# Optimization experiments

Measured on AMD Instinct MI355X. Metric: run time of the kernel, lower is better.

The kernel has to match this reference:

```python
import jax, jax.numpy as jnp
import numpy as np

N = 50000
E = 800000
F_IN = 512
H = 128
K = 10
ALPHA = 0.1
EPS = 1e-5  # BatchNorm eps


def setup_inputs() -> dict:
    key = jax.random.key(0)
    ks = jax.random.split(key, 16)
    x = jax.random.normal(ks[0], (N, F_IN), dtype=jnp.float32)
    edge_index = jax.random.randint(ks[1], (2, E), 0, N, dtype=jnp.int64)
    # Linear weights (xavier-ish scale)
    W1 = jax.random.normal(ks[2], (F_IN, H), dtype=jnp.float32) * (1.0 / np.sqrt(F_IN))
    b1 = jnp.zeros((H,), dtype=jnp.float32)
    W2 = jax.random.normal(ks[3], (H, H), dtype=jnp.float32) * (1.0 / np.sqrt(H))
    b2 = jnp.zeros((H,), dtype=jnp.float32)
    # BatchNorm (eval mode: running stats)
    gamma1 = jnp.ones((H,), dtype=jnp.float32)
    beta1 = jnp.zeros((H,), dtype=jnp.float32)
    mean1 = jax.random.normal(ks[4], (H,), dtype=jnp.float32) * 0.1
    var1 = jax.random.uniform(ks[5], (H,), dtype=jnp.float32) + 0.5
    gamma2 = jnp.ones((H,), dtype=jnp.float32)
    beta2 = jnp.zeros((H,), dtype=jnp.float32)
    mean2 = jax.random.normal(ks[6], (H,), dtype=jnp.float32) * 0.1
    var2 = jax.random.uniform(ks[7], (H,), dtype=jnp.float32) + 0.5
    return {
        "x": x, "edge_index": edge_index,
        "W1": W1, "b1": b1, "gamma1": gamma1, "beta1": beta1, "mean1": mean1, "var1": var1,
        "W2": W2, "b2": b2, "gamma2": gamma2, "beta2": beta2, "mean2": mean2, "var2": var2,
    }


def _bn_eval(h, gamma, beta, mean, var):
    return (h - mean) * jax.lax.rsqrt(var + EPS) * gamma + beta


def _appnp_prop(h, edge_index):
    # add self loops
    loop = jnp.arange(N, dtype=edge_index.dtype)
    src = jnp.concatenate([edge_index[0], loop])
    dst = jnp.concatenate([edge_index[1], loop])
    # symmetric GCN normalization: deg^{-1/2}[src] * deg^{-1/2}[dst]
    deg = jax.ops.segment_sum(jnp.ones_like(src, dtype=h.dtype), dst, num_segments=N)
    dinv = jax.lax.rsqrt(jnp.maximum(deg, 1.0))
    norm = dinv[src] * dinv[dst]  # [E+N]
    h0 = h

    def step(carry, _):
        msg = carry[src] * norm[:, None]                    # [E+N, H]
        agg = jax.ops.segment_sum(msg, dst, num_segments=N)  # [N, H]
        return (1.0 - ALPHA) * agg + ALPHA * h0, None

    out, _ = jax.lax.scan(step, h, None, length=K)
    return out


def reference(x, edge_index, W1, b1, gamma1, beta1, mean1, var1,
              W2, b2, gamma2, beta2, mean2, var2):
    h = jax.nn.relu(x @ W1 + b1)
    h = _bn_eval(h, gamma1, beta1, mean1, var1)
    # dropout inactive (eval mode)
    h = h @ W2 + b2
    h = _bn_eval(h, gamma2, beta2, mean2, var2)
    return _appnp_prop(h, edge_index)
```

## Files before the change

kernel.cpp:

```cpp
#include <hip/hip_runtime.h>

#define ALPHA_F 0.1f
#define EPS_F   1e-5f

typedef float    f32x4 __attribute__((ext_vector_type(4)));
typedef _Float16 h16x8 __attribute__((ext_vector_type(8)));
typedef _Float16 h16x2 __attribute__((ext_vector_type(2)));

__device__ __forceinline__ void gll16(const void* g, void* l)
{
    __builtin_amdgcn_global_load_lds(
        (const __attribute__((address_space(1))) void*)g,
        (__attribute__((address_space(3))) void*)l, 16, 0, 0);
}

__device__ __forceinline__ int pad_cnt(int d) { return (d + 8) & ~7; }

__global__ void convert_wstg(const float* __restrict__ W,
                             _Float16* __restrict__ Wstg, int K)
{
    int idx = blockIdx.x * 256 + threadIdx.x;
    if (idx < K * 128) {
        int k = idx >> 7, n = idx & 127;
        int i = k >> 5, kg = (k >> 3) & 3, j = k & 7;
        Wstg[(size_t)i * 4096 + (kg * 128 + n) * 8 + j] = (_Float16)W[idx];
    }
}

template<bool A_HALF, bool OUT_HALF>
__global__ __launch_bounds__(256) void gemm_stage_bn(
    const void* __restrict__ Av,
    const _Float16* __restrict__ Wstg,
    const float* __restrict__ bias,
    const float* __restrict__ gamma, const float* __restrict__ beta,
    const float* __restrict__ mean,  const float* __restrict__ var,
    void* __restrict__ outv, int M, int K, int do_relu)
{
    __shared__ __align__(16) char Abuf[2][8192];
    __shared__ __align__(16) char Wbuf[2][8192];

    const int t   = threadIdx.x;
    const int w   = t >> 6;
    const int l   = t & 63;
    const int l15 = l & 15;
    const int lk  = l >> 4;
    const int bm  = blockIdx.x * 64;
    const int nk  = K >> 5;
    const int row = w * 16 + l15;

    f32x4 acc[8];
#pragma unroll
    for (int f = 0; f < 8; ++f) acc[f] = (f32x4){0.f, 0.f, 0.f, 0.f};

    auto stage = [&](int buf, int i) {
        const char* wsrc = (const char*)Wstg + (size_t)i * 8192;
#pragma unroll
        for (int c = 0; c < 2; ++c) {
            const int base = w * 128 + c * 64;
            gll16(wsrc + (size_t)(base + l) * 16, &Wbuf[buf][base * 16]);
        }
        if (A_HALF) {
            const int base = w * 64;
            const int sl   = base + l;
            const int r    = sl >> 2;
            const int ch   = (sl & 3) ^ (r & 3);
            int gr = bm + r; gr = (gr < M) ? gr : (M - 1);
            const char* src = (const char*)Av + ((size_t)gr * K + i * 32) * 2
                              + (size_t)ch * 16;
            gll16(src, &Abuf[buf][base * 16]);
        } else {
#pragma unroll
            for (int c = 0; c < 2; ++c) {
                const int base = w * 128 + c * 64;
                const int sl   = base + l;
                const int r    = sl >> 3;
                const int ch   = (sl & 7) ^ (r & 7);
                int gr = bm + r; gr = (gr < M) ? gr : (M - 1);
                const char* src = (const char*)Av + ((size_t)gr * K + i * 32) * 4
                                  + (size_t)ch * 16;
                gll16(src, &Abuf[buf][base * 16]);
            }
        }
    };

    auto compute = [&](int buf) {
        h16x8 a;
        if (A_HALF) {
            a = *(const h16x8*)&Abuf[buf][(row * 4 + (lk ^ (row & 3))) * 16];
        } else {
            f32x4 a0 = *(const f32x4*)&Abuf[buf][(row * 8 + ((2 * lk)     ^ (row & 7))) * 16];
            f32x4 a1 = *(const f32x4*)&Abuf[buf][(row * 8 + ((2 * lk + 1) ^ (row & 7))) * 16];
#pragma unroll
            for (int j = 0; j < 4; ++j) {
                a[j]     = (_Float16)a0[j];
                a[4 + j] = (_Float16)a1[j];
            }
        }
#pragma unroll
        for (int f = 0; f < 8; ++f) {
            h16x8 b = *(const h16x8*)&Wbuf[buf][(lk * 128 + f * 16 + l15) * 16];
            acc[f] = __builtin_amdgcn_mfma_f32_16x16x32_f16(a, b, acc[f], 0, 0, 0);
        }
    };

    stage(0, 0);
    for (int i = 0; i < nk; ++i) {
        __syncthreads();
        if (i + 1 < nk) stage((i + 1) & 1, i + 1);
        compute(i & 1);
    }

#pragma unroll
    for (int f = 0; f < 8; ++f) {
        const int col = f * 16 + l15;
        float s  = gamma[col] * rsqrtf(var[col] + EPS_F);
        float sh = beta[col] - mean[col] * s;
        float bb = bias[col];
#pragma unroll
        for (int rr = 0; rr < 4; ++rr) {
            int rg = bm + w * 16 + lk * 4 + rr;
            if (rg < M) {
                float v = acc[f][rr] + bb;
                if (do_relu) v = fmaxf(v, 0.f);
                v = v * s + sh;
                if (OUT_HALF) ((_Float16*)outv)[(size_t)rg * 128 + col] = (_Float16)v;
                else          ((float*)outv)[(size_t)rg * 128 + col]    = v;
            }
        }
    }
}

__global__ void count_deg(const int* __restrict__ dst, int E, int* __restrict__ deg)
{
    int e = blockIdx.x * 256 + threadIdx.x;
    if (e < E) atomicAdd(&deg[dst[e]], 1);
}

__global__ __launch_bounds__(256) void scan_block_sums(
    const int* __restrict__ deg, int* __restrict__ bsum, int N)
{
    __shared__ int sh[256];
    const int t  = threadIdx.x;
    const int i0 = blockIdx.x * 1024 + t * 4;
    int s = 0;
    if (i0 + 3 < N) {
        int4 d4 = *(const int4*)(deg + i0);
        s = pad_cnt(d4.x) + pad_cnt(d4.y) + pad_cnt(d4.z) + pad_cnt(d4.w);
    } else {
#pragma unroll
        for (int j = 0; j < 4; ++j)
            if (i0 + j < N) s += pad_cnt(deg[i0 + j]);
    }
    sh[t] = s;
    __syncthreads();
#pragma unroll
    for (int d = 128; d > 0; d >>= 1) {
        if (t < d) sh[t] += sh[t + d];
        __syncthreads();
    }
    if (t == 0) bsum[blockIdx.x] = sh[0];
}

__global__ __launch_bounds__(256) void scan_offsets(
    const int* __restrict__ deg, const int* __restrict__ bsum,
    int* __restrict__ offs, int* __restrict__ cursor,
    float* __restrict__ dinv, int N, int B)
{
    __shared__ int sh[256];
    __shared__ int sbase;
    const int b = blockIdx.x, t = threadIdx.x;

    int v = (t < b && t < B) ? bsum[t] : 0;
    sh[t] = v;
    __syncthreads();
#pragma unroll
    for (int d = 128; d > 0; d >>= 1) {
        if (t < d) sh[t] += sh[t + d];
        __syncthreads();
    }
    if (t == 0) sbase = sh[0];
    __syncthreads();

    const int i0 = b * 1024 + t * 4;
    int c[4], s = 0;
#pragma unroll
    for (int j = 0; j < 4; ++j) {
        int i = i0 + j;
        c[j] = (i < N) ? pad_cnt(deg[i]) : 0;
        s += c[j];
    }
    sh[t] = s;
    __syncthreads();
    for (int d = 1; d < 256; d <<= 1) {
        int o = (t >= d) ? sh[t - d] : 0;
        __syncthreads();
        sh[t] += o;
        __syncthreads();
    }
    int run = sbase + sh[t] - s;
#pragma unroll
    for (int j = 0; j < 4; ++j) {
        int i = i0 + j;
        if (i < N) {
            offs[i]   = run;
            cursor[i] = run;
            dinv[i]   = rsqrtf((float)(deg[i] + 1));
            run += c[j];
        }
    }
    if (b == B - 1 && t == 255) offs[N] = run;
}

__global__ void scatter_csr(const int* __restrict__ src, const int* __restrict__ dst,
                            int E, const float* __restrict__ dinv,
                            int* __restrict__ cursor, int2* __restrict__ csr)
{
    int e = blockIdx.x * 256 + threadIdx.x;
    if (e < E) {
        int s = src[e], d = dst[e];
        int pos = atomicAdd(&cursor[d], 1);
        csr[pos] = make_int2(s, __float_as_int(dinv[s] * dinv[d]));
    }
}

__global__ void fill_self_pad(const int* __restrict__ offs, const int* __restrict__ deg,
                              const float* __restrict__ dinv,
                              int2* __restrict__ csr, int N)
{
    int i = blockIdx.x * 256 + threadIdx.x;
    if (i < N) {
        int base = offs[i], d = deg[i], end = offs[i + 1];
        float di = dinv[i];
        csr[base + d] = make_int2(i, __float_as_int(di * di));
        for (int p = base + d + 1; p < end; ++p)
            csr[p] = make_int2(i, 0);
    }
}

#define NWAVES 8192

__global__ __launch_bounds__(256) void appnp_step(
    const _Float16* __restrict__ cur, const _Float16* __restrict__ h0,
    const int* __restrict__ offs, const int2* __restrict__ csr,
    _Float16* __restrict__ nxt, float* __restrict__ fout, int N)
{
    const int wv0  = __builtin_amdgcn_readfirstlane(
                        (int)((blockIdx.x * 256u + threadIdx.x) >> 6));
    const int lane = (int)(threadIdx.x & 63u);
    const int g    = lane >> 4;
    const int fl   = (lane & 15) * 8;

    for (int i = wv0; i < N; i += NWAVES) {
        int e   = offs[i];
        int end = offs[i + 1];

        h16x2 acc[4];
#pragma unroll
        for (int j = 0; j < 4; ++j) acc[j] = (h16x2){(_Float16)0, (_Float16)0};

        int4 m = *(const int4*)(csr + e + 2 * g);
        h16x8 vA = *(const h16x8*)(cur + (size_t)m.x * 128 + fl);
        h16x8 vB = *(const h16x8*)(cur + (size_t)m.z * 128 + fl);

        for (e += 8; e < end; e += 8) {
            int4 m2 = *(const int4*)(csr + e + 2 * g);
            h16x8 vA2 = *(const h16x8*)(cur + (size_t)m2.x * 128 + fl);
            h16x8 vB2 = *(const h16x8*)(cur + (size_t)m2.z * 128 + fl);
            _Float16 ha = (_Float16)__int_as_float(m.y);
            _Float16 hb = (_Float16)__int_as_float(m.w);
            h16x2 wa = (h16x2){ha, ha}, wb = (h16x2){hb, hb};
#pragma unroll
            for (int j = 0; j < 4; ++j) {
                h16x2 va = (h16x2){vA[2 * j], vA[2 * j + 1]};
                h16x2 vb = (h16x2){vB[2 * j], vB[2 * j + 1]};
                acc[j] = __builtin_elementwise_fma(wa, va, acc[j]);
                acc[j] = __builtin_elementwise_fma(wb, vb, acc[j]);
            }
            m = m2; vA = vA2; vB = vB2;
        }
        {
            _Float16 ha = (_Float16)__int_as_float(m.y);
            _Float16 hb = (_Float16)__int_as_float(m.w);
            h16x2 wa = (h16x2){ha, ha}, wb = (h16x2){hb, hb};
#pragma unroll
            for (int j = 0; j < 4; ++j) {
                h16x2 va = (h16x2){vA[2 * j], vA[2 * j + 1]};
                h16x2 vb = (h16x2){vB[2 * j], vB[2 * j + 1]};
                acc[j] = __builtin_elementwise_fma(wa, va, acc[j]);
                acc[j] = __builtin_elementwise_fma(wb, vb, acc[j]);
            }
        }

        float o[8];
#pragma unroll
        for (int j = 0; j < 4; ++j) {
            o[2 * j]     = (float)acc[j][0];
            o[2 * j + 1] = (float)acc[j][1];
        }
#pragma unroll
        for (int j = 0; j < 8; ++j) {
            o[j] += __shfl_xor(o[j], 16);
            o[j] += __shfl_xor(o[j], 32);
        }

        if (lane < 16) {
            h16x8 hv = *(const h16x8*)(h0 + (size_t)i * 128 + fl);
#pragma unroll
            for (int j = 0; j < 8; ++j)
                o[j] = ALPHA_F * (float)hv[j] + (1.f - ALPHA_F) * o[j];
            if (fout) {
                f32x4 o0, o1;
#pragma unroll
                for (int j = 0; j < 4; ++j) { o0[j] = o[j]; o1[j] = o[4 + j]; }
                *(f32x4*)(fout + (size_t)i * 128 + fl)     = o0;
                *(f32x4*)(fout + (size_t)i * 128 + fl + 4) = o1;
            } else {
                h16x8 o16;
#pragma unroll
                for (int j = 0; j < 8; ++j) o16[j] = (_Float16)o[j];
                *(h16x8*)(nxt + (size_t)i * 128 + fl) = o16;
            }
        }
    }
}

static inline size_t align_up(size_t x) { return (x + 255) & ~(size_t)255; }

extern "C" void kernel_launch(void* const* d_in, const int* in_sizes, int n_in,
                              void* d_out, int out_size, void* d_ws, size_t ws_size,
                              hipStream_t stream)
{
    const float* x   = (const float*)d_in[0];
    const int*   ei  = (const int*)d_in[1];
    const float* W1  = (const float*)d_in[2];
    const float* b1  = (const float*)d_in[3];
    const float* g1  = (const float*)d_in[4];
    const float* be1 = (const float*)d_in[5];
    const float* m1  = (const float*)d_in[6];
    const float* v1  = (const float*)d_in[7];
    const float* W2  = (const float*)d_in[8];
    const float* b2  = (const float*)d_in[9];
    const float* g2  = (const float*)d_in[10];
    const float* be2 = (const float*)d_in[11];
    const float* m2  = (const float*)d_in[12];
    const float* v2  = (const float*)d_in[13];

    const int N = in_sizes[0] / 512;
    const int E = in_sizes[1] / 2;
    const int* src = ei;
    const int* dst = ei + E;
    const int CSR_CAP = E + 8 * N;
    const int NB = (N + 1023) / 1024;

    char* ws = (char*)d_ws;
    size_t off = 0;
    _Float16* hAh = (_Float16*)(ws + off); off += align_up((size_t)N * 128 * 2);
    _Float16* h0h = (_Float16*)(ws + off); off += align_up((size_t)N * 128 * 2);
    _Float16* p0  = (_Float16*)(ws + off); off += align_up((size_t)N * 128 * 2);
    _Float16* p1  = (_Float16*)(ws + off); off += align_up((size_t)N * 128 * 2);
    int*    deg  = (int*)(ws + off);    off += align_up((size_t)N * 4);
    float*  dinv = (float*)(ws + off);  off += align_up((size_t)N * 4);
    int*    offs = (int*)(ws + off);    off += align_up((size_t)(N + 1) * 4);
    int*    curs = (int*)(ws + off);    off += align_up((size_t)N * 4);
    int*    bsum = (int*)(ws + off);    off += align_up((size_t)256 * 4);
    int2*   csr  = (int2*)(ws + off);   off += align_up((size_t)CSR_CAP * 8);
    _Float16* w1s = (_Float16*)(ws + off); off += align_up((size_t)512 * 128 * 2);
    _Float16* w2s = (_Float16*)(ws + off); off += align_up((size_t)128 * 128 * 2);

    hipMemsetAsync(deg, 0, (size_t)N * 4, stream);
    count_deg<<<(E + 255) / 256, 256, 0, stream>>>(dst, E, deg);
    scan_block_sums<<<NB, 256, 0, stream>>>(deg, bsum, N);
    scan_offsets<<<NB, 256, 0, stream>>>(deg, bsum, offs, curs, dinv, N, NB);
    scatter_csr<<<(E + 255) / 256, 256, 0, stream>>>(src, dst, E, dinv, curs, csr);
    fill_self_pad<<<(N + 255) / 256, 256, 0, stream>>>(offs, deg, dinv, csr, N);

    convert_wstg<<<(512 * 128 + 255) / 256, 256, 0, stream>>>(W1, w1s, 512);
    convert_wstg<<<(128 * 128 + 255) / 256, 256, 0, stream>>>(W2, w2s, 128);

    gemm_stage_bn<false, true><<<(N + 63) / 64, 256, 0, stream>>>(
        x, w1s, b1, g1, be1, m1, v1, hAh, N, 512, 1);
    gemm_stage_bn<true, true><<<(N + 63) / 64, 256, 0, stream>>>(
        hAh, w2s, b2, g2, be2, m2, v2, h0h, N, 128, 0);

    const _Float16* cur = h0h;
    for (int k = 0; k < 10; ++k) {
        _Float16* nxt = (k & 1) ? p1 : p0;
        float* fo = (k == 9) ? (float*)d_out : nullptr;
        appnp_step<<<NWAVES / 4, 256, 0, stream>>>(
            cur, h0h, offs, csr, nxt, fo, N);
        cur = nxt;
    }

    (void)n_in; (void)out_size; (void)ws_size;
}
```

Before: 430.0 us.

## Store propagation features as packed 12-bit fixed-point to cut gather bandwidth

```diff
diff --git a/kernel.cpp b/kernel.cpp
--- a/kernel.cpp
+++ b/kernel.cpp
@@ -2,10 +2,11 @@
 
 #define ALPHA_F 0.1f
 #define EPS_F   1e-5f
+#define INV256  0.00390625f
 
 typedef float    f32x4 __attribute__((ext_vector_type(4)));
 typedef _Float16 h16x8 __attribute__((ext_vector_type(8)));
-typedef _Float16 h16x2 __attribute__((ext_vector_type(2)));
+typedef int      i32x3 __attribute__((ext_vector_type(3)));
 
 __device__ __forceinline__ void gll16(const void* g, void* l)
 {
@@ -15,6 +16,51 @@
 }
 
 __device__ __forceinline__ int pad_cnt(int d) { return (d + 8) & ~7; }
+
+__device__ __forceinline__ void pack12(const float* o, unsigned* d)
+{
+    int q[8];
+#pragma unroll
+    for (int j = 0; j < 8; ++j) {
+        float x = fminf(fmaxf(o[j] * 256.f, -2047.f), 2047.f);
+        q[j] = (int)lrintf(x) & 0xFFF;
+    }
+    d[0] = (unsigned)q[0] | ((unsigned)q[1] << 12) | ((unsigned)q[2] << 24);
+    d[1] = ((unsigned)q[2] >> 8) | ((unsigned)q[3] << 4)
+         | ((unsigned)q[4] << 16) | ((unsigned)q[5] << 28);
+    d[2] = ((unsigned)q[5] >> 4) | ((unsigned)q[6] << 8) | ((unsigned)q[7] << 20);
+}
+
+__device__ __forceinline__ void unpack12(unsigned d0, unsigned d1, unsigned d2,
+                                         float* f)
+{
+    f[0] = (float)(((int)(d0 << 20)) >> 20);
+    f[1] = (float)(((int)(d0 << 8))  >> 20);
+    unsigned u2 = (d0 >> 24) | (d1 << 8);
+    f[2] = (float)(((int)(u2 << 20)) >> 20);
+    f[3] = (float)(((int)(d1 << 16)) >> 20);
+    f[4] = (float)(((int)(d1 << 4))  >> 20);
+    unsigned u5 = (d1 >> 28) | (d2 << 4);
+    f[5] = (float)(((int)(u5 << 20)) >> 20);
+    f[6] = (float)(((int)(d2 << 12)) >> 20);
+    f[7] = (float)(((int)d2) >> 20);
+}
+
+__global__ void pack_rows(const _Float16* __restrict__ src,
+                          unsigned* __restrict__ dst, int total)
+{
+    int idx = blockIdx.x * 256 + threadIdx.x;
+    if (idx < total) {
+        h16x8 v = *(const h16x8*)(src + (size_t)idx * 8);
+        float o[8];
+#pragma unroll
+        for (int j = 0; j < 8; ++j) o[j] = (float)v[j];
+        unsigned d[3];
+        pack12(o, d);
+        unsigned* p = dst + (size_t)idx * 3;
+        p[0] = d[0]; p[1] = d[1]; p[2] = d[2];
+    }
+}
 
 __global__ void convert_wstg(const float* __restrict__ W,
                              _Float16* __restrict__ Wstg, int K)
@@ -239,86 +285,80 @@
 
 #define NWAVES 8192
 
-__global__ __launch_bounds__(256) void appnp_step(
-    const _Float16* __restrict__ cur, const _Float16* __restrict__ h0,
+__global__ __launch_bounds__(256) void appnp_step_q(
+    const unsigned* __restrict__ cur, const _Float16* __restrict__ h0,
     const int* __restrict__ offs, const int2* __restrict__ csr,
-    _Float16* __restrict__ nxt, float* __restrict__ fout, int N)
+    unsigned* __restrict__ nxt, float* __restrict__ fout, int N)
 {
     const int wv0  = __builtin_amdgcn_readfirstlane(
                         (int)((blockIdx.x * 256u + threadIdx.x) >> 6));
     const int lane = (int)(threadIdx.x & 63u);
     const int g    = lane >> 4;
-    const int fl   = (lane & 15) * 8;
+    const int sl   = lane & 15;
+    const int dw   = sl * 3;
 
     for (int i = wv0; i < N; i += NWAVES) {
         int e   = offs[i];
         int end = offs[i + 1];
 
-        h16x2 acc[4];
-#pragma unroll
-        for (int j = 0; j < 4; ++j) acc[j] = (h16x2){(_Float16)0, (_Float16)0};
-
-        int4 m = *(const int4*)(csr + e + 2 * g);
-        h16x8 vA = *(const h16x8*)(cur + (size_t)m.x * 128 + fl);
-        h16x8 vB = *(const h16x8*)(cur + (size_t)m.z * 128 + fl);
+        float acc[8];
+#pragma unroll
+        for (int j = 0; j < 8; ++j) acc[j] = 0.f;
+
+        int4  m = *(const int4*)(csr + e + 2 * g);
+        i32x3 a = *(const i32x3*)(cur + (size_t)m.x * 48 + dw);
+        i32x3 b = *(const i32x3*)(cur + (size_t)m.z * 48 + dw);
 
         for (e += 8; e < end; e += 8) {
-            int4 m2 = *(const int4*)(csr + e + 2 * g);
-            h16x8 vA2 = *(const h16x8*)(cur + (size_t)m2.x * 128 + fl);
-            h16x8 vB2 = *(const h16x8*)(cur + (size_t)m2.z * 128 + fl);
-            _Float16 ha = (_Float16)__int_as_float(m.y);
-            _Float16 hb = (_Float16)__int_as_float(m.w);
-            h16x2 wa = (h16x2){ha, ha}, wb = (h16x2){hb, hb};
-#pragma unroll
-            for (int j = 0; j < 4; ++j) {
-                h16x2 va = (h16x2){vA[2 * j], vA[2 * j + 1]};
-                h16x2 vb = (h16x2){vB[2 * j], vB[2 * j + 1]};
-                acc[j] = __builtin_elementwise_fma(wa, va, acc[j]);
-                acc[j] = __builtin_elementwise_fma(wb, vb, acc[j]);
-            }
-            m = m2; vA = vA2; vB = vB2;
+            int4  m2 = *(const int4*)(csr + e + 2 * g);
+            i32x3 a2 = *(const i32x3*)(cur + (size_t)m2.x * 48 + dw);
+            i32x3 b2 = *(const i32x3*)(cur + (size_t)m2.z * 48 + dw);
+
+            float wA = __int_as_float(m.y) * INV256;
+            float wB = __int_as_float(m.w) * INV256;
+            float fa[8], fb[8];
+            unpack12((unsigned)a[0], (unsigned)a[1], (unsigned)a[2], fa);
+            unpack12((unsigned)b[0], (unsigned)b[1], (unsigned)b[2], fb);
+#pragma unroll
+            for (int j = 0; j < 8; ++j)
+                acc[j] = fmaf(wA, fa[j], fmaf(wB, fb[j], acc[j]));
+
+            m = m2; a = a2; b = b2;
         }
         {
-            _Float16 ha = (_Float16)__int_as_float(m.y);
-            _Float16 hb = (_Float16)__int_as_float(m.w);
-            h16x2 wa = (h16x2){ha, ha}, wb = (h16x2){hb, hb};
-#pragma unroll
-            for (int j = 0; j < 4; ++j) {
-                h16x2 va = (h16x2){vA[2 * j], vA[2 * j + 1]};
-                h16x2 vb = (h16x2){vB[2 * j], vB[2 * j + 1]};
-                acc[j] = __builtin_elementwise_fma(wa, va, acc[j]);
-                acc[j] = __builtin_elementwise_fma(wb, vb, acc[j]);
-            }
-        }
-
-        float o[8];
-#pragma unroll
-        for (int j = 0; j < 4; ++j) {
-            o[2 * j]     = (float)acc[j][0];
-            o[2 * j + 1] = (float)acc[j][1];
-        }
+            float wA = __int_as_float(m.y) * INV256;
+            float wB = __int_as_float(m.w) * INV256;
+            float fa[8], fb[8];
+            unpack12((unsigned)a[0], (unsigned)a[1], (unsigned)a[2], fa);
+            unpack12((unsigned)b[0], (unsigned)b[1], (unsigned)b[2], fb);
+#pragma unroll
+            for (int j = 0; j < 8; ++j)
+                acc[j] = fmaf(wA, fa[j], fmaf(wB, fb[j], acc[j]));
+        }
+
 #pragma unroll
         for (int j = 0; j < 8; ++j) {
-            o[j] += __shfl_xor(o[j], 16);
-            o[j] += __shfl_xor(o[j], 32);
+            acc[j] += __shfl_xor(acc[j], 16);
+            acc[j] += __shfl_xor(acc[j], 32);
         }
 
         if (lane < 16) {
-            h16x8 hv = *(const h16x8*)(h0 + (size_t)i * 128 + fl);
+            h16x8 hv = *(const h16x8*)(h0 + (size_t)i * 128 + sl * 8);
+            float o[8];
 #pragma unroll
             for (int j = 0; j < 8; ++j)
-                o[j] = ALPHA_F * (float)hv[j] + (1.f - ALPHA_F) * o[j];
+                o[j] = ALPHA_F * (float)hv[j] + (1.f - ALPHA_F) * acc[j];
             if (fout) {
                 f32x4 o0, o1;
 #pragma unroll
                 for (int j = 0; j < 4; ++j) { o0[j] = o[j]; o1[j] = o[4 + j]; }
-                *(f32x4*)(fout + (size_t)i * 128 + fl)     = o0;
-                *(f32x4*)(fout + (size_t)i * 128 + fl + 4) = o1;
+                *(f32x4*)(fout + (size_t)i * 128 + sl * 8)     = o0;
+                *(f32x4*)(fout + (size_t)i * 128 + sl * 8 + 4) = o1;
             } else {
-                h16x8 o16;
-#pragma unroll
-                for (int j = 0; j < 8; ++j) o16[j] = (_Float16)o[j];
-                *(h16x8*)(nxt + (size_t)i * 128 + fl) = o16;
+                unsigned d[3];
+                pack12(o, d);
+                unsigned* p = nxt + (size_t)i * 48 + dw;
+                p[0] = d[0]; p[1] = d[1]; p[2] = d[2];
             }
         }
     }
@@ -356,8 +396,9 @@
     size_t off = 0;
     _Float16* hAh = (_Float16*)(ws + off); off += align_up((size_t)N * 128 * 2);
     _Float16* h0h = (_Float16*)(ws + off); off += align_up((size_t)N * 128 * 2);
-    _Float16* p0  = (_Float16*)(ws + off); off += align_up((size_t)N * 128 * 2);
-    _Float16* p1  = (_Float16*)(ws + off); off += align_up((size_t)N * 128 * 2);
+    unsigned* q0  = (unsigned*)(ws + off); off += align_up((size_t)N * 48 * 4);
+    unsigned* q1  = (unsigned*)(ws + off); off += align_up((size_t)N * 48 * 4);
+    unsigned* q2  = (unsigned*)(ws + off); off += align_up((size_t)N * 48 * 4);
     int*    deg  = (int*)(ws + off);    off += align_up((size_t)N * 4);
     float*  dinv = (float*)(ws + off);  off += align_up((size_t)N * 4);
     int*    offs = (int*)(ws + off);    off += align_up((size_t)(N + 1) * 4);
@@ -382,11 +423,13 @@
     gemm_stage_bn<true, true><<<(N + 63) / 64, 256, 0, stream>>>(
         hAh, w2s, b2, g2, be2, m2, v2, h0h, N, 128, 0);
 
-    const _Float16* cur = h0h;
+    pack_rows<<<(N * 16 + 255) / 256, 256, 0, stream>>>(h0h, q0, N * 16);
+
+    const unsigned* cur = q0;
     for (int k = 0; k < 10; ++k) {
-        _Float16* nxt = (k & 1) ? p1 : p0;
+        unsigned* nxt = (k & 1) ? q2 : q1;
         float* fo = (k == 9) ? (float*)d_out : nullptr;
-        appnp_step<<<NWAVES / 4, 256, 0, stream>>>(
+        appnp_step_q<<<NWAVES / 4, 256, 0, stream>>>(
             cur, h0h, offs, csr, nxt, fo, N);
         cur = nxt;
     }
```

New measurement: 457.3 us. 1.06x slower.

## Pack CSR entries into 32-bit words and fuse edge scatter into GEMM1 launch

Applied to the files above, without the earlier changes.

```diff
diff --git a/kernel.cpp b/kernel.cpp
--- a/kernel.cpp
+++ b/kernel.cpp
@@ -15,6 +15,13 @@
 }
 
 __device__ __forceinline__ int pad_cnt(int d) { return (d + 8) & ~7; }
+
+__device__ __forceinline__ unsigned pack_csr(int s, float w)
+{
+    _Float16 h = (_Float16)w;
+    return (unsigned)(s & 0xFFFF)
+         | ((unsigned)__builtin_bit_cast(unsigned short, h) << 16);
+}
 
 __global__ void convert_wstg(const float* __restrict__ W,
                              _Float16* __restrict__ Wstg, int K)
@@ -27,14 +34,13 @@
     }
 }
 
-template<bool A_HALF, bool OUT_HALF>
-__global__ __launch_bounds__(256) void gemm_stage_bn(
-    const void* __restrict__ Av,
+__global__ __launch_bounds__(256) void gemm_stage_bn_h(
+    const _Float16* __restrict__ Ah,
     const _Float16* __restrict__ Wstg,
     const float* __restrict__ bias,
     const float* __restrict__ gamma, const float* __restrict__ beta,
     const float* __restrict__ mean,  const float* __restrict__ var,
-    void* __restrict__ outv, int M, int K, int do_relu)
+    _Float16* __restrict__ outh, int M, int K)
 {
     __shared__ __align__(16) char Abuf[2][8192];
     __shared__ __align__(16) char Wbuf[2][8192];
@@ -59,43 +65,18 @@
             const int base = w * 128 + c * 64;
             gll16(wsrc + (size_t)(base + l) * 16, &Wbuf[buf][base * 16]);
         }
-        if (A_HALF) {
-            const int base = w * 64;
-            const int sl   = base + l;
-            const int r    = sl >> 2;
-            const int ch   = (sl & 3) ^ (r & 3);
-            int gr = bm + r; gr = (gr < M) ? gr : (M - 1);
-            const char* src = (const char*)Av + ((size_t)gr * K + i * 32) * 2
-                              + (size_t)ch * 16;
-            gll16(src, &Abuf[buf][base * 16]);
-        } else {
-#pragma unroll
-            for (int c = 0; c < 2; ++c) {
-                const int base = w * 128 + c * 64;
-                const int sl   = base + l;
-                const int r    = sl >> 3;
-                const int ch   = (sl & 7) ^ (r & 7);
-                int gr = bm + r; gr = (gr < M) ? gr : (M - 1);
-                const char* src = (const char*)Av + ((size_t)gr * K + i * 32) * 4
-                                  + (size_t)ch * 16;
-                gll16(src, &Abuf[buf][base * 16]);
-            }
-        }
+        const int base = w * 64;
+        const int sl   = base + l;
+        const int r    = sl >> 2;
+        const int ch   = (sl & 3) ^ (r & 3);
+        int gr = bm + r; gr = (gr < M) ? gr : (M - 1);
+        const char* src = (const char*)Ah + ((size_t)gr * K + i * 32) * 2
+                          + (size_t)ch * 16;
+        gll16(src, &Abuf[buf][base * 16]);
     };
 
     auto compute = [&](int buf) {
-        h16x8 a;
-        if (A_HALF) {
-            a = *(const h16x8*)&Abuf[buf][(row * 4 + (lk ^ (row & 3))) * 16];
-        } else {
-            f32x4 a0 = *(const f32x4*)&Abuf[buf][(row * 8 + ((2 * lk)     ^ (row & 7))) * 16];
-            f32x4 a1 = *(const f32x4*)&Abuf[buf][(row * 8 + ((2 * lk + 1) ^ (row & 7))) * 16];
-#pragma unroll
-            for (int j = 0; j < 4; ++j) {
-                a[j]     = (_Float16)a0[j];
-                a[4 + j] = (_Float16)a1[j];
-            }
-        }
+        h16x8 a = *(const h16x8*)&Abuf[buf][(row * 4 + (lk ^ (row & 3))) * 16];
 #pragma unroll
         for (int f = 0; f < 8; ++f) {
             h16x8 b = *(const h16x8*)&Wbuf[buf][(lk * 128 + f * 16 + l15) * 16];
@@ -119,12 +100,105 @@
 #pragma unroll
         for (int rr = 0; rr < 4; ++rr) {
             int rg = bm + w * 16 + lk * 4 + rr;
+            if (rg < M)
+                outh[(size_t)rg * 128 + col] =
+                    (_Float16)((acc[f][rr] + bb) * s + sh);
+        }
+    }
+}
+
+__global__ __launch_bounds__(256) void fused_gemm1_scatter(
+    const float* __restrict__ Af,
+    const _Float16* __restrict__ Wstg,
+    const float* __restrict__ bias,
+    const float* __restrict__ gamma, const float* __restrict__ beta,
+    const float* __restrict__ mean,  const float* __restrict__ var,
+    _Float16* __restrict__ outh, int M, int K, int GB,
+    const int* __restrict__ src, const int* __restrict__ dst, int E,
+    const float* __restrict__ dinv, int* __restrict__ cursor,
+    unsigned* __restrict__ csr4)
+{
+    __shared__ __align__(16) char Abuf[2][8192];
+    __shared__ __align__(16) char Wbuf[2][8192];
+
+    if (blockIdx.x >= GB) {
+        int e = (blockIdx.x - GB) * 256 + threadIdx.x;
+        if (e < E) {
+            int s = src[e], d = dst[e];
+            int pos = atomicAdd(&cursor[d], 1);
+            csr4[pos] = pack_csr(s, dinv[s] * dinv[d]);
+        }
+        return;
+    }
+
+    const int t   = threadIdx.x;
+    const int w   = t >> 6;
+    const int l   = t & 63;
+    const int l15 = l & 15;
+    const int lk  = l >> 4;
+    const int bm  = blockIdx.x * 64;
+    const int nk  = K >> 5;
+    const int row = w * 16 + l15;
+
+    f32x4 acc[8];
+#pragma unroll
+    for (int f = 0; f < 8; ++f) acc[f] = (f32x4){0.f, 0.f, 0.f, 0.f};
+
+    auto stage = [&](int buf, int i) {
+        const char* wsrc = (const char*)Wstg + (size_t)i * 8192;
+#pragma unroll
+        for (int c = 0; c < 2; ++c) {
+            const int base = w * 128 + c * 64;
+            gll16(wsrc + (size_t)(base + l) * 16, &Wbuf[buf][base * 16]);
+        }
+#pragma unroll
+        for (int c = 0; c < 2; ++c) {
+            const int base = w * 128 + c * 64;
+            const int sl   = base + l;
+            const int r    = sl >> 3;
+            const int ch   = (sl & 7) ^ (r & 7);
+            int gr = bm + r; gr = (gr < M) ? gr : (M - 1);
+            const char* srcp = (const char*)Af + ((size_t)gr * K + i * 32) * 4
+                               + (size_t)ch * 16;
+            gll16(srcp, &Abuf[buf][base * 16]);
+        }
+    };
+
+    auto compute = [&](int buf) {
+        f32x4 a0 = *(const f32x4*)&Abuf[buf][(row * 8 + ((2 * lk)     ^ (row & 7))) * 16];
+        f32x4 a1 = *(const f32x4*)&Abuf[buf][(row * 8 + ((2 * lk + 1) ^ (row & 7))) * 16];
+        h16x8 a;
+#pragma unroll
+        for (int j = 0; j < 4; ++j) {
+            a[j]     = (_Float16)a0[j];
+            a[4 + j] = (_Float16)a1[j];
+        }
+#pragma unroll
+        for (int f = 0; f < 8; ++f) {
+            h16x8 b = *(const h16x8*)&Wbuf[buf][(lk * 128 + f * 16 + l15) * 16];
+            acc[f] = __builtin_amdgcn_mfma_f32_16x16x32_f16(a, b, acc[f], 0, 0, 0);
+        }
+    };
+
+    stage(0, 0);
+    for (int i = 0; i < nk; ++i) {
+        __syncthreads();
+        if (i + 1 < nk) stage((i + 1) & 1, i + 1);
+        compute(i & 1);
+    }
+
+#pragma unroll
+    for (int f = 0; f < 8; ++f) {
+        const int col = f * 16 + l15;
+        float s  = gamma[col] * rsqrtf(var[col] + EPS_F);
+        float sh = beta[col] - mean[col] * s;
+        float bb = bias[col];
+#pragma unroll
+        for (int rr = 0; rr < 4; ++rr) {
+            int rg = bm + w * 16 + lk * 4 + rr;
             if (rg < M) {
-                float v = acc[f][rr] + bb;
-                if (do_relu) v = fmaxf(v, 0.f);
-                v = v * s + sh;
-                if (OUT_HALF) ((_Float16*)outv)[(size_t)rg * 128 + col] = (_Float16)v;
-                else          ((float*)outv)[(size_t)rg * 128 + col]    = v;
+                float v = fmaxf(acc[f][rr] + bb, 0.f);
+                outh[(size_t)rg * 128 + col] = (_Float16)(v * s + sh);
             }
         }
     }
@@ -211,29 +285,17 @@
     if (b == B - 1 && t == 255) offs[N] = run;
 }
 
-__global__ void scatter_csr(const int* __restrict__ src, const int* __restrict__ dst,
-                            int E, const float* __restrict__ dinv,
-                            int* __restrict__ cursor, int2* __restrict__ csr)
-{
-    int e = blockIdx.x * 256 + threadIdx.x;
-    if (e < E) {
-        int s = src[e], d = dst[e];
-        int pos = atomicAdd(&cursor[d], 1);
-        csr[pos] = make_int2(s, __float_as_int(dinv[s] * dinv[d]));
-    }
-}
-
 __global__ void fill_self_pad(const int* __restrict__ offs, const int* __restrict__ deg,
                               const float* __restrict__ dinv,
-                              int2* __restrict__ csr, int N)
+                              unsigned* __restrict__ csr4, int N)
 {
     int i = blockIdx.x * 256 + threadIdx.x;
     if (i < N) {
         int base = offs[i], d = deg[i], end = offs[i + 1];
         float di = dinv[i];
-        csr[base + d] = make_int2(i, __float_as_int(di * di));
+        csr4[base + d] = pack_csr(i, di * di);
         for (int p = base + d + 1; p < end; ++p)
-            csr[p] = make_int2(i, 0);
+            csr4[p] = pack_csr(i, 0.f);
     }
 }
 
@@ -241,7 +303,7 @@
 
 __global__ __launch_bounds__(256) void appnp_step(
     const _Float16* __restrict__ cur, const _Float16* __restrict__ h0,
-    const int* __restrict__ offs, const int2* __restrict__ csr,
+    const int* __restrict__ offs, const unsigned* __restrict__ csr4,
     _Float16* __restrict__ nxt, float* __restrict__ fout, int N)
 {
     const int wv0  = __builtin_amdgcn_readfirstlane(
@@ -258,16 +320,16 @@
 #pragma unroll
         for (int j = 0; j < 4; ++j) acc[j] = (h16x2){(_Float16)0, (_Float16)0};
 
-        int4 m = *(const int4*)(csr + e + 2 * g);
-        h16x8 vA = *(const h16x8*)(cur + (size_t)m.x * 128 + fl);
-        h16x8 vB = *(const h16x8*)(cur + (size_t)m.z * 128 + fl);
+        uint2 m = *(const uint2*)(csr4 + e + 2 * g);
+        h16x8 vA = *(const h16x8*)(cur + (size_t)(m.x & 0xFFFFu) * 128 + fl);
+        h16x8 vB = *(const h16x8*)(cur + (size_t)(m.y & 0xFFFFu) * 128 + fl);
 
         for (e += 8; e < end; e += 8) {
-            int4 m2 = *(const int4*)(csr + e + 2 * g);
-            h16x8 vA2 = *(const h16x8*)(cur + (size_t)m2.x * 128 + fl);
-            h16x8 vB2 = *(const h16x8*)(cur + (size_t)m2.z * 128 + fl);
-            _Float16 ha = (_Float16)__int_as_float(m.y);
-            _Float16 hb = (_Float16)__int_as_float(m.w);
+            uint2 m2 = *(const uint2*)(csr4 + e + 2 * g);
+            h16x8 vA2 = *(const h16x8*)(cur + (size_t)(m2.x & 0xFFFFu) * 128 + fl);
+            h16x8 vB2 = *(const h16x8*)(cur + (size_t)(m2.y & 0xFFFFu) * 128 + fl);
+            _Float16 ha = __builtin_bit_cast(_Float16, (unsigned short)(m.x >> 16));
+            _Float16 hb = __builtin_bit_cast(_Float16, (unsigned short)(m.y >> 16));
             h16x2 wa = (h16x2){ha, ha}, wb = (h16x2){hb, hb};
 #pragma unroll
             for (int j = 0; j < 4; ++j) {
@@ -279,8 +341,8 @@
             m = m2; vA = vA2; vB = vB2;
         }
         {
-            _Float16 ha = (_Float16)__int_as_float(m.y);
-            _Float16 hb = (_Float16)__int_as_float(m.w);
+            _Float16 ha = __builtin_bit_cast(_Float16, (unsigned short)(m.x >> 16));
+            _Float16 hb = __builtin_bit_cast(_Float16, (unsigned short)(m.y >> 16));
             h16x2 wa = (h16x2){ha, ha}, wb = (h16x2){hb, hb};
 #pragma unroll
             for (int j = 0; j < 4; ++j) {
@@ -351,6 +413,8 @@
     const int* dst = ei + E;
     const int CSR_CAP = E + 8 * N;
     const int NB = (N + 1023) / 1024;
+    const int GB = (N + 63) / 64;
+    const int SB = (E + 255) / 256;
 
     char* ws = (char*)d_ws;
     size_t off = 0;
@@ -363,7 +427,7 @@
     int*    offs = (int*)(ws + off);    off += align_up((size_t)(N + 1) * 4);
     int*    curs = (int*)(ws + off);    off += align_up((size_t)N * 4);
     int*    bsum = (int*)(ws + off);    off += align_up((size_t)256 * 4);
-    int2*   csr  = (int2*)(ws + off);   off += align_up((size_t)CSR_CAP * 8);
+    unsigned* csr4 = (unsigned*)(ws + off); off += align_up((size_t)CSR_CAP * 4);
     _Float16* w1s = (_Float16*)(ws + off); off += align_up((size_t)512 * 128 * 2);
     _Float16* w2s = (_Float16*)(ws + off); off += align_up((size_t)128 * 128 * 2);
 
@@ -371,23 +435,24 @@
     count_deg<<<(E + 255) / 256, 256, 0, stream>>>(dst, E, deg);
     scan_block_sums<<<NB, 256, 0, stream>>>(deg, bsum, N);
     scan_offsets<<<NB, 256, 0, stream>>>(deg, bsum, offs, curs, dinv, N, NB);
-    scatter_csr<<<(E + 255) / 256, 256, 0, stream>>>(src, dst, E, dinv, curs, csr);
-    fill_self_pad<<<(N + 255) / 256, 256, 0, stream>>>(offs, deg, dinv, csr, N);
 
     convert_wstg<<<(512 * 128 + 255) / 256, 256, 0, stream>>>(W1, w1s, 512);
     convert_wstg<<<(128 * 128 + 255) / 256, 256, 0, stream>>>(W2, w2s, 128);
 
-    gemm_stage_bn<false, true><<<(N + 63) / 64, 256, 0, stream>>>(
-        x, w1s, b1, g1, be1, m1, v1, hAh, N, 512, 1);
-    gemm_stage_bn<true, true><<<(N + 63) / 64, 256, 0, stream>>>(
-        hAh, w2s, b2, g2, be2, m2, v2, h0h, N, 128, 0);
+    fused_gemm1_scatter<<<GB + SB, 256, 0, stream>>>(
+        x, w1s, b1, g1, be1, m1, v1, hAh, N, 512, GB,
+        src, dst, E, dinv, curs, csr4);
+
+    fill_self_pad<<<(N + 255) / 256, 256, 0, stream>>>(offs, deg, dinv, csr4, N);
+    gemm_stage_bn_h<<<GB, 256, 0, stream>>>(
+        hAh, w2s, b2, g2, be2, m2, v2, h0h, N, 128);
 
     const _Float16* cur = h0h;
     for (int k = 0; k < 10; ++k) {
         _Float16* nxt = (k & 1) ? p1 : p0;
         float* fo = (k == 9) ? (float*)d_out : nullptr;
         appnp_step<<<NWAVES / 4, 256, 0, stream>>>(
-            cur, h0h, offs, csr, nxt, fo, N);
+            cur, h0h, offs, csr4, nxt, fo, N);
         cur = nxt;
     }
 
```

Measured after the change: 405.0 us. 5.8% less time.
